# Kernel optimization log

Measured on AMD Instinct MI355X. Metric: run time of the kernel, lower is better.

Reference implementation:

```python
import jax, jax.numpy as jnp
import numpy as np
from jax import lax

N = 32768      # total nodes (8 graphs x 4096)
E = 262144     # edges (avg degree 8)
B = 8          # graphs in batch
TW = 25        # time window
H = 128        # hidden features
L = 6          # GNN layers
NV = 1         # n_variables (pos_t only)
SD = 1         # spatial dim
TMAX, TMIN, RES_T = 4.0, 0.0, 250.0
BD_LOW, BD_UP = 0.0, 16.0
EPS = 1e-5


def swish(x):
    return x * jax.nn.sigmoid(x)


def setup_inputs() -> dict:
    key = jax.random.key(0)
    ks = jax.random.split(key, 32)
    s = 0.05
    u = jax.random.normal(ks[0], (N, TW), jnp.float32)
    pos_t = jax.random.uniform(ks[1], (N, 1), jnp.float32) * TMAX
    pos_x = jax.random.uniform(ks[2], (N, 1), jnp.float32) * BD_UP
    pos = jnp.concatenate([pos_t, pos_x], axis=-1)
    edge_index = jax.random.randint(ks[3], (2, E), 0, N, jnp.int64)
    batch = jnp.repeat(jnp.arange(B, dtype=jnp.int64), N // B)
    d_in = TW + SD + NV          # 27
    d_msg = 2 * H + TW + SD + NV  # 282
    d_upd = H + H + NV            # 257
    We1 = jax.random.normal(ks[4], (d_in, H), jnp.float32) * s
    be1 = jnp.zeros((H,), jnp.float32)
    We2 = jax.random.normal(ks[5], (H, H), jnp.float32) * s
    be2 = jnp.zeros((H,), jnp.float32)
    Wm1 = jax.random.normal(ks[6], (L, d_msg, H), jnp.float32) * s
    bm1 = jnp.zeros((L, H), jnp.float32)
    Wm2 = jax.random.normal(ks[7], (L, H, H), jnp.float32) * s
    bm2 = jnp.zeros((L, H), jnp.float32)
    Wu1 = jax.random.normal(ks[8], (L, d_upd, H), jnp.float32) * s
    bu1 = jnp.zeros((L, H), jnp.float32)
    Wu2 = jax.random.normal(ks[9], (L, H, H), jnp.float32) * s
    bu2 = jnp.zeros((L, H), jnp.float32)
    Wc1 = jax.random.normal(ks[10], (8, 1, 16), jnp.float32) * s  # OIH
    bc1 = jnp.zeros((8,), jnp.float32)
    Wc2 = jax.random.normal(ks[11], (1, 8, 14), jnp.float32) * s
    bc2 = jnp.zeros((1,), jnp.float32)
    return dict(u=u, pos=pos, edge_index=edge_index, batch=batch,
                We1=We1, be1=be1, We2=We2, be2=be2,
                Wm1=Wm1, bm1=bm1, Wm2=Wm2, bm2=bm2,
                Wu1=Wu1, bu1=bu1, Wu2=Wu2, bu2=bu2,
                Wc1=Wc1, bc1=bc1, Wc2=Wc2, bc2=bc2)


def _mpnn(u, pos, edge_index, batch, We1, be1, We2, be2,
          Wm1, bm1, Wm2, bm2, Wu1, bu1, Wu2, bu2, Wc1, bc1, Wc2, bc2):
    src = edge_index[0]   # j (source)
    tgt = edge_index[1]   # i (target)
    pos_t = pos[:, 0:1] / TMAX
    pos_x = (pos[:, 1:] - BD_LOW) / (BD_UP - BD_LOW)
    variables = pos_t  # eq_variables empty -> only normalized time

    node_input = jnp.concatenate([u, pos_x, variables], axis=-1)  # [N, 27]
    h = swish(node_input @ We1 + be1)
    h = swish(h @ We2 + be2)

    # in-degree for scatter-mean (empty targets -> 0 like PyG mean)
    cnt = jnp.zeros((N,), jnp.float32).at[tgt].add(1.0)
    cnt = jnp.maximum(cnt, 1.0)[:, None]
    # per-graph node counts for InstanceNorm
    gcnt = jax.ops.segment_sum(jnp.ones((N,), jnp.float32), batch, num_segments=B)[:, None]

    u_diff_e = u[tgt] - u[src]          # [E, TW]
    p_diff_e = pos_x[tgt] - pos_x[src]  # [E, SD]
    var_i_e = variables[tgt]            # [E, NV]

    for l in range(L):
        # message: gather -> MLP per edge
        m_in = jnp.concatenate([h[tgt], h[src], u_diff_e, p_diff_e, var_i_e], axis=-1)  # [E, 282]
        msg = swish(m_in @ Wm1[l] + bm1[l])
        msg = swish(msg @ Wm2[l] + bm2[l])
        # scatter-mean aggregate onto targets
        agg = jax.ops.segment_sum(msg, tgt, num_segments=N) / cnt  # [N, H]
        # node update MLP, residual (in_features == out_features)
        up = jnp.concatenate([h, agg, variables], axis=-1)  # [N, 257]
        up = swish(up @ Wu1[l] + bu1[l])
        up = swish(up @ Wu2[l] + bu2[l])
        h = h + up
        # InstanceNorm per graph (no affine), biased variance
        mean = jax.ops.segment_sum(h, batch, num_segments=B) / gcnt      # [B, H]
        sq = jax.ops.segment_sum(h * h, batch, num_segments=B) / gcnt    # [B, H]
        var = sq - mean * mean
        h = (h - mean[batch]) / jnp.sqrt(var[batch] + EPS)

    # output CNN: tw=25 branch
    hc = h[:, None, :]  # [N, 1, 128]
    dn = ('NCH', 'OIH', 'NCH')
    c = lax.conv_general_dilated(hc, Wc1, (3,), 'VALID', dimension_numbers=dn) + bc1[None, :, None]
    c = swish(c)
    c = lax.conv_general_dilated(c, Wc2, (1,), 'VALID', dimension_numbers=dn) + bc2[None, :, None]
    diff = c[:, 0, :]  # [N, 25]

    dt = (TMAX - TMIN) / RES_T
    dt_cum = jnp.arange(1, TW + 1, dtype=jnp.float32) * dt  # cumsum of ones*dt
    out = u[:, -1:] + dt_cum[None, :] * diff
    return out


def reference(u, pos, edge_index, batch, We1, be1, We2, be2,
              Wm1, bm1, Wm2, bm2, Wu1, bu1, Wu2, bu2, Wc1, bc1, Wc2, bc2):
    return _mpnn(u, pos, edge_index, batch, We1, be1, We2, be2,
                 Wm1, bm1, Wm2, bm2, Wu1, bu1, Wu2, bu2, Wc1, bc1, Wc2, bc2)
```

## Files before the change

kernel.cpp:

```cpp
#include <hip/hip_runtime.h>
#include <stdint.h>

#define N_NODES 32768
#define N_EDGES 262144
#define NB 8
#define TW 25

typedef __attribute__((ext_vector_type(8))) short short8;
typedef __attribute__((ext_vector_type(4))) float floatx4;

__device__ __forceinline__ float swishf(float x) { return x / (1.0f + __expf(-x)); }

__device__ __forceinline__ unsigned short f2bf(float x) {
    union { float f; unsigned u; } v; v.f = x;
    unsigned r = v.u + 0x7FFFu + ((v.u >> 16) & 1u);
    return (unsigned short)(r >> 16);
}
__device__ __forceinline__ float bf2f(unsigned short b) {
    union { unsigned u; float f; } v; v.u = ((unsigned)b) << 16; return v.f;
}

__global__ void init_kernel(const float* __restrict__ pos,
                            float* __restrict__ posx, float* __restrict__ post) {
    int i = blockIdx.x * 256 + threadIdx.x;
    if (i < N_NODES) {
        post[i] = pos[i * 2 + 0] * 0.25f;
        posx[i] = pos[i * 2 + 1] * 0.0625f;
    }
}

__global__ void deg_kernel(const int* __restrict__ tgt, int* __restrict__ deg) {
    int i = blockIdx.x * 256 + threadIdx.x;
    if (i < N_EDGES) atomicAdd(&deg[tgt[i]], 1);
}

__global__ __launch_bounds__(1024) void scan_kernel(const int* __restrict__ deg,
                                                    int* __restrict__ cursor) {
    __shared__ int ps[1024];
    int t = threadIdx.x;
    int base = t * 32;
    int tot = 0;
    for (int i = 0; i < 32; ++i) tot += deg[base + i];
    ps[t] = tot;
    __syncthreads();
    for (int off = 1; off < 1024; off <<= 1) {
        int v = (t >= off) ? ps[t - off] : 0;
        __syncthreads();
        ps[t] += v;
        __syncthreads();
    }
    int run = ps[t] - tot;
    for (int i = 0; i < 32; ++i) {
        cursor[base + i] = run;
        run += deg[base + i];
    }
}

__global__ void scatter_kernel(const int* __restrict__ src, const int* __restrict__ tgt,
                               int* __restrict__ cursor,
                               int* __restrict__ src_s, int* __restrict__ tgt_s) {
    int i = blockIdx.x * 256 + threadIdx.x;
    if (i < N_EDGES) {
        int tg = tgt[i];
        int p = atomicAdd(&cursor[tg], 1);
        src_s[p] = src[i];
        tgt_s[p] = tg;
    }
}

__global__ __launch_bounds__(256) void ediff_kernel(
    const float* __restrict__ u, const float* __restrict__ posx,
    const float* __restrict__ post,
    const int* __restrict__ src_s, const int* __restrict__ tgt_s,
    unsigned short* __restrict__ ediff)
{
    int e = blockIdx.x * 256 + threadIdx.x;
    if (e >= N_EDGES) return;
    int s = src_s[e], g = tgt_s[e];
    unsigned short buf[32];
    #pragma unroll
    for (int k = 0; k < 25; ++k)
        buf[k] = f2bf(u[(size_t)g * 25 + k] - u[(size_t)s * 25 + k]);
    buf[25] = f2bf(posx[g] - posx[s]);
    buf[26] = f2bf(post[g]);
    #pragma unroll
    for (int k = 27; k < 32; ++k) buf[k] = 0;
    #pragma unroll
    for (int j = 0; j < 4; ++j)
        *(short8*)(ediff + (size_t)e * 32 + j * 8) = *(short8*)&buf[j * 8];
}

__global__ __launch_bounds__(256) void pack_kernel(const float* __restrict__ W,
                                                   unsigned short* __restrict__ Wp,
                                                   int Kreal, int Kc, int total) {
    int id = blockIdx.x * 256 + threadIdx.x;
    if (id >= total) return;
    int lane = id & 63;
    int t8 = (id >> 6) & 7;
    int rest = id >> 9;
    int c = rest % Kc;
    int l = rest / Kc;
    int n = t8 * 16 + (lane & 15);
    int kb = c * 32 + (lane >> 4) * 8;
    short8 v;
    #pragma unroll
    for (int j = 0; j < 8; ++j) {
        int k = kb + j;
        float x = (k < Kreal) ? W[((size_t)l * Kreal + k) * 128 + n] : 0.f;
        v[j] = (short)f2bf(x);
    }
    *(short8*)(Wp + (size_t)id * 8) = v;
}

__global__ __launch_bounds__(256) void encoder_kernel(
    const float* __restrict__ u, const float* __restrict__ posx,
    const float* __restrict__ post,
    const float* __restrict__ We1, const float* __restrict__ be1,
    const float* __restrict__ We2, const float* __restrict__ be2,
    float* __restrict__ h, unsigned short* __restrict__ h_bf,
    float* __restrict__ agg)
{
    __shared__ __align__(16) float As[64 * 36];
    __shared__ __align__(16) float Ws[32 * 128];
    __shared__ __align__(16) float Ms[64 * 128];

    int t = threadIdx.x;
    int n0 = blockIdx.x * 64;
    int rg = t >> 5, cg = t & 31;

    {
        int r = t & 63, cseg = t >> 6;
        float4 z = make_float4(0.f, 0.f, 0.f, 0.f);
        #pragma unroll
        for (int j = 0; j < 8; ++j)
            *(float4*)(agg + (size_t)(n0 + r) * 128 + cseg * 32 + j * 4) = z;
    }

    float acc[8][4] = {};
    {
        int kk = t >> 3, cb = (t & 7) * 16;
        #pragma unroll
        for (int j = 0; j < 4; ++j) {
            float4 w = make_float4(0.f, 0.f, 0.f, 0.f);
            if (kk < 27) w = *(const float4*)&We1[kk * 128 + cb + j * 4];
            *(float4*)&Ws[kk * 128 + cb + j * 4] = w;
        }
        int el = t >> 2, kb = (t & 3) * 8, n = n0 + el;
        float v[8];
        #pragma unroll
        for (int j = 0; j < 8; ++j) {
            int k = kb + j;
            float x = 0.f;
            if (k < 25) x = u[n * 25 + k];
            else if (k == 25) x = posx[n];
            else if (k == 26) x = post[n];
            v[j] = x;
        }
        #pragma unroll
        for (int j = 0; j < 8; j += 4)
            *(float4*)&As[el * 36 + kb + j] = make_float4(v[j], v[j+1], v[j+2], v[j+3]);
        __syncthreads();
        #pragma unroll 4
        for (int kk2 = 0; kk2 < 32; ++kk2) {
            float4 b = *(const float4*)&Ws[kk2 * 128 + cg * 4];
            float a[8];
            #pragma unroll
            for (int i = 0; i < 8; ++i) a[i] = As[(rg * 8 + i) * 36 + kk2];
            #pragma unroll
            for (int i = 0; i < 8; ++i) {
                acc[i][0] += a[i] * b.x; acc[i][1] += a[i] * b.y;
                acc[i][2] += a[i] * b.z; acc[i][3] += a[i] * b.w;
            }
        }
        __syncthreads();
    }
    {
        float4 b1 = *(const float4*)&be1[cg * 4];
        #pragma unroll
        for (int i = 0; i < 8; ++i) {
            float4 m;
            m.x = swishf(acc[i][0] + b1.x);
            m.y = swishf(acc[i][1] + b1.y);
            m.z = swishf(acc[i][2] + b1.z);
            m.w = swishf(acc[i][3] + b1.w);
            *(float4*)&Ms[(rg * 8 + i) * 128 + cg * 4] = m;
        }
        __syncthreads();
    }
    float acc2[8][4] = {};
    for (int k0 = 0; k0 < 128; k0 += 32) {
        int kk = t >> 3, cb = (t & 7) * 16;
        #pragma unroll
        for (int j = 0; j < 4; ++j)
            *(float4*)&Ws[kk * 128 + cb + j * 4] =
                *(const float4*)&We2[(k0 + kk) * 128 + cb + j * 4];
        __syncthreads();
        #pragma unroll 4
        for (int kk2 = 0; kk2 < 32; ++kk2) {
            float4 b = *(const float4*)&Ws[kk2 * 128 + cg * 4];
            float a[8];
            #pragma unroll
            for (int i = 0; i < 8; ++i) a[i] = Ms[(rg * 8 + i) * 128 + (k0 + kk2)];
            #pragma unroll
            for (int i = 0; i < 8; ++i) {
                acc2[i][0] += a[i] * b.x; acc2[i][1] += a[i] * b.y;
                acc2[i][2] += a[i] * b.z; acc2[i][3] += a[i] * b.w;
            }
        }
        __syncthreads();
    }
    {
        float4 b2 = *(const float4*)&be2[cg * 4];
        #pragma unroll
        for (int i = 0; i < 8; ++i) {
            int n = n0 + rg * 8 + i;
            float4 o;
            o.x = swishf(acc2[i][0] + b2.x);
            o.y = swishf(acc2[i][1] + b2.y);
            o.z = swishf(acc2[i][2] + b2.z);
            o.w = swishf(acc2[i][3] + b2.w);
            *(float4*)&h[(size_t)n * 128 + cg * 4] = o;
            unsigned short* hb = h_bf + (size_t)n * 128 + cg * 4;
            uint2 pk;
            pk.x = (unsigned)f2bf(o.x) | ((unsigned)f2bf(o.y) << 16);
            pk.y = (unsigned)f2bf(o.z) | ((unsigned)f2bf(o.w) << 16);
            *(uint2*)hb = pk;
        }
    }
}

__global__ __launch_bounds__(256, 4) void message_kernel(
    const unsigned short* __restrict__ h_bf,
    const unsigned short* __restrict__ ediff,
    const int* __restrict__ src_s, const int* __restrict__ tgt_s,
    const unsigned short* __restrict__ W1p, const float* __restrict__ b1,
    const unsigned short* __restrict__ W2p, const float* __restrict__ b2,
    float* __restrict__ agg, float* __restrict__ stats)
{
    __shared__ __align__(16) unsigned short SH[64 * 296];
    __shared__ int tgtS[64];
    unsigned short* Msh = SH;
    unsigned short* Cs  = SH + 9216;

    int t = threadIdx.x;
    int e0 = blockIdx.x * 64;
    if (blockIdx.x == 0) {
        float4 z = make_float4(0.f, 0.f, 0.f, 0.f);
        *(float4*)&stats[t * 8] = z;
        *(float4*)&stats[t * 8 + 4] = z;
    }
    if (t < 64) tgtS[t] = tgt_s[e0 + t];

    {
        int r = t & 63, cseg = t >> 6;
        int g = tgt_s[e0 + r], s = src_s[e0 + r];
        const short8* hg = (const short8*)(h_bf + (size_t)g * 128);
        const short8* hs = (const short8*)(h_bf + (size_t)s * 128);
        #pragma unroll
        for (int j = 0; j < 4; ++j) {
            int chunk = cseg * 4 + j;
            *(short8*)(SH + r * 296 + chunk * 8)       = hg[chunk];
            *(short8*)(SH + r * 296 + 128 + chunk * 8) = hs[chunk];
        }
        *(short8*)(SH + r * 296 + 256 + cseg * 8) =
            *(const short8*)(ediff + (size_t)(e0 + r) * 32 + cseg * 8);
    }
    __syncthreads();

    int w = t >> 6, lane = t & 63, q = lane >> 4, m = lane & 15;
    int t80 = 2 * w, t81 = 2 * w + 1;

    floatx4 acc0[4] = {}, acc1[4] = {};
    #pragma unroll
    for (int c = 0; c < 9; ++c) {
        short8 b0 = *(const short8*)(W1p + ((size_t)(c * 8 + t80) * 64 + lane) * 8);
        short8 b1f = *(const short8*)(W1p + ((size_t)(c * 8 + t81) * 64 + lane) * 8);
        #pragma unroll
        for (int g2 = 0; g2 < 4; ++g2) {
            short8 a = *(const short8*)(SH + (g2 * 16 + m) * 296 + c * 32 + q * 8);
            acc0[g2] = __builtin_amdgcn_mfma_f32_16x16x32_bf16(a, b0, acc0[g2], 0, 0, 0);
            acc1[g2] = __builtin_amdgcn_mfma_f32_16x16x32_bf16(a, b1f, acc1[g2], 0, 0, 0);
        }
    }
    __syncthreads();

    {
        float bv0 = b1[t80 * 16 + m], bv1 = b1[t81 * 16 + m];
        #pragma unroll
        for (int g2 = 0; g2 < 4; ++g2) {
            #pragma unroll
            for (int r = 0; r < 4; ++r) {
                int row = g2 * 16 + q * 4 + r;
                Msh[row * 136 + t80 * 16 + m] = f2bf(swishf(acc0[g2][r] + bv0));
                Msh[row * 136 + t81 * 16 + m] = f2bf(swishf(acc1[g2][r] + bv1));
            }
        }
    }
    __syncthreads();

    floatx4 acc2a[4] = {}, acc2b[4] = {};
    #pragma unroll
    for (int c = 0; c < 4; ++c) {
        short8 b0 = *(const short8*)(W2p + ((size_t)(c * 8 + t80) * 64 + lane) * 8);
        short8 b1f = *(const short8*)(W2p + ((size_t)(c * 8 + t81) * 64 + lane) * 8);
        #pragma unroll
        for (int g2 = 0; g2 < 4; ++g2) {
            short8 a = *(const short8*)(Msh + (g2 * 16 + m) * 136 + c * 32 + q * 8);
            acc2a[g2] = __builtin_amdgcn_mfma_f32_16x16x32_bf16(a, b0, acc2a[g2], 0, 0, 0);
            acc2b[g2] = __builtin_amdgcn_mfma_f32_16x16x32_bf16(a, b1f, acc2b[g2], 0, 0, 0);
        }
    }
    {
        float bv0 = b2[t80 * 16 + m], bv1 = b2[t81 * 16 + m];
        #pragma unroll
        for (int g2 = 0; g2 < 4; ++g2) {
            #pragma unroll
            for (int r = 0; r < 4; ++r) {
                int row = g2 * 16 + q * 4 + r;
                Cs[row * 132 + t80 * 16 + m] = f2bf(swishf(acc2a[g2][r] + bv0));
                Cs[row * 132 + t81 * 16 + m] = f2bf(swishf(acc2b[g2][r] + bv1));
            }
        }
    }
    __syncthreads();

    {
        int col = t & 127, half = t >> 7;
        int r0 = half * 32;
        float run = 0.f;
        int prev = tgtS[r0];
        bool atStart = true;
        for (int i = 0; i < 32; ++i) {
            int tg = tgtS[r0 + i];
            if (tg != prev) {
                float* dst = &agg[(size_t)prev * 128 + col];
                if (atStart) atomicAdd(dst, run);
                else *dst = run;
                run = 0.f; prev = tg; atStart = false;
            }
            run += bf2f(Cs[(r0 + i) * 132 + col]);
        }
        atomicAdd(&agg[(size_t)prev * 128 + col], run);
    }
}

__global__ __launch_bounds__(256, 2) void update_kernel(
    float* __restrict__ h, const unsigned short* __restrict__ h_bf,
    float* __restrict__ agg, const int* __restrict__ deg,
    const float* __restrict__ post,
    const unsigned short* __restrict__ W1p, const float* __restrict__ b1,
    const unsigned short* __restrict__ W2p, const float* __restrict__ b2,
    float* __restrict__ stats)
{
    __shared__ __align__(16) unsigned short SH[64 * 296];
    unsigned short* Msh = SH;

    int t = threadIdx.x;
    int n0 = blockIdx.x * 64;

    {
        int r = t & 63, cseg = t >> 6;
        int n = n0 + r;
        const short8* hn = (const short8*)(h_bf + (size_t)n * 128);
        #pragma unroll
        for (int j = 0; j < 4; ++j) {
            int chunk = cseg * 4 + j;
            *(short8*)(SH + r * 296 + chunk * 8) = hn[chunk];
        }
        float ic = 1.0f / fmaxf((float)deg[n], 1.0f);
        #pragma unroll
        for (int j = 0; j < 4; ++j) {
            int unit = cseg * 4 + j;
            const float* ap = agg + (size_t)n * 128 + unit * 8;
            float4 v0 = *(const float4*)ap;
            float4 v1 = *(const float4*)(ap + 4);
            short8 a;
            a[0] = (short)f2bf(v0.x * ic); a[1] = (short)f2bf(v0.y * ic);
            a[2] = (short)f2bf(v0.z * ic); a[3] = (short)f2bf(v0.w * ic);
            a[4] = (short)f2bf(v1.x * ic); a[5] = (short)f2bf(v1.y * ic);
            a[6] = (short)f2bf(v1.z * ic); a[7] = (short)f2bf(v1.w * ic);
            *(short8*)(SH + r * 296 + 128 + unit * 8) = a;
        }
        short8 z;
        #pragma unroll
        for (int k = 0; k < 8; ++k) z[k] = 0;
        if (cseg == 0) z[0] = (short)f2bf(post[n]);
        *(short8*)(SH + r * 296 + 256 + cseg * 8) = z;
    }
    __syncthreads();

    int w = t >> 6, lane = t & 63, q = lane >> 4, m = lane & 15;
    int t80 = 2 * w, t81 = 2 * w + 1;

    floatx4 acc0[4] = {}, acc1[4] = {};
    #pragma unroll
    for (int c = 0; c < 9; ++c) {
        short8 b0 = *(const short8*)(W1p + ((size_t)(c * 8 + t80) * 64 + lane) * 8);
        short8 b1f = *(const short8*)(W1p + ((size_t)(c * 8 + t81) * 64 + lane) * 8);
        #pragma unroll
        for (int g2 = 0; g2 < 4; ++g2) {
            short8 a = *(const short8*)(SH + (g2 * 16 + m) * 296 + c * 32 + q * 8);
            acc0[g2] = __builtin_amdgcn_mfma_f32_16x16x32_bf16(a, b0, acc0[g2], 0, 0, 0);
            acc1[g2] = __builtin_amdgcn_mfma_f32_16x16x32_bf16(a, b1f, acc1[g2], 0, 0, 0);
        }
    }
    __syncthreads();

    {
        float bv0 = b1[t80 * 16 + m], bv1 = b1[t81 * 16 + m];
        #pragma unroll
        for (int g2 = 0; g2 < 4; ++g2) {
            #pragma unroll
            for (int r = 0; r < 4; ++r) {
                int row = g2 * 16 + q * 4 + r;
                Msh[row * 136 + t80 * 16 + m] = f2bf(swishf(acc0[g2][r] + bv0));
                Msh[row * 136 + t81 * 16 + m] = f2bf(swishf(acc1[g2][r] + bv1));
            }
        }
    }
    __syncthreads();

    floatx4 acc2a[4] = {}, acc2b[4] = {};
    #pragma unroll
    for (int c = 0; c < 4; ++c) {
        short8 b0 = *(const short8*)(W2p + ((size_t)(c * 8 + t80) * 64 + lane) * 8);
        short8 b1f = *(const short8*)(W2p + ((size_t)(c * 8 + t81) * 64 + lane) * 8);
        #pragma unroll
        for (int g2 = 0; g2 < 4; ++g2) {
            short8 a = *(const short8*)(Msh + (g2 * 16 + m) * 136 + c * 32 + q * 8);
            acc2a[g2] = __builtin_amdgcn_mfma_f32_16x16x32_bf16(a, b0, acc2a[g2], 0, 0, 0);
            acc2b[g2] = __builtin_amdgcn_mfma_f32_16x16x32_bf16(a, b1f, acc2b[g2], 0, 0, 0);
        }
    }

    int bidx = n0 >> 12;
    int col0 = t80 * 16 + m, col1 = t81 * 16 + m;
    float bv0 = b2[col0], bv1 = b2[col1];
    float s0 = 0.f, s20 = 0.f, s1 = 0.f, s21 = 0.f;
    #pragma unroll
    for (int g2 = 0; g2 < 4; ++g2) {
        #pragma unroll
        for (int r = 0; r < 4; ++r) {
            int row = g2 * 16 + q * 4 + r;
            size_t i0 = (size_t)(n0 + row) * 128 + col0;
            size_t i1 = (size_t)(n0 + row) * 128 + col1;
            float hv0 = h[i0] + swishf(acc2a[g2][r] + bv0);
            float hv1 = h[i1] + swishf(acc2b[g2][r] + bv1);
            h[i0] = hv0; h[i1] = hv1;
            s0 += hv0; s20 += hv0 * hv0;
            s1 += hv1; s21 += hv1 * hv1;
        }
    }
    s0  += __shfl_xor(s0, 16);  s0  += __shfl_xor(s0, 32);
    s20 += __shfl_xor(s20, 16); s20 += __shfl_xor(s20, 32);
    s1  += __shfl_xor(s1, 16);  s1  += __shfl_xor(s1, 32);
    s21 += __shfl_xor(s21, 16); s21 += __shfl_xor(s21, 32);
    if (q == 0) {
        atomicAdd(&stats[bidx * 128 + col0], s0);
        atomicAdd(&stats[(NB + bidx) * 128 + col0], s20);
        atomicAdd(&stats[bidx * 128 + col1], s1);
        atomicAdd(&stats[(NB + bidx) * 128 + col1], s21);
    }
    {
        int r = t & 63, cseg = t >> 6;
        float4 z = make_float4(0.f, 0.f, 0.f, 0.f);
        #pragma unroll
        for (int j = 0; j < 8; ++j)
            *(float4*)(agg + (size_t)(n0 + r) * 128 + cseg * 32 + j * 4) = z;
    }
}

__global__ __launch_bounds__(256) void norm_kernel(float* __restrict__ h,
                                                   unsigned short* __restrict__ h_bf,
                                                   const float* __restrict__ stats) {
    size_t id = (size_t)blockIdx.x * 256 + threadIdx.x;
    int n = (int)(id >> 5), c4 = (int)(id & 31) * 4;
    int b = n >> 12;
    float4 mn = *(const float4*)&stats[b * 128 + c4];
    float4 sq = *(const float4*)&stats[(NB + b) * 128 + c4];
    float4 v = *(const float4*)&h[(size_t)n * 128 + c4];
    float4 r;
    float m0 = mn.x * (1.f / 4096.f), m1 = mn.y * (1.f / 4096.f);
    float m2 = mn.z * (1.f / 4096.f), m3 = mn.w * (1.f / 4096.f);
    r.x = (v.x - m0) * rsqrtf(sq.x * (1.f / 4096.f) - m0 * m0 + 1e-5f);
    r.y = (v.y - m1) * rsqrtf(sq.y * (1.f / 4096.f) - m1 * m1 + 1e-5f);
    r.z = (v.z - m2) * rsqrtf(sq.z * (1.f / 4096.f) - m2 * m2 + 1e-5f);
    r.w = (v.w - m3) * rsqrtf(sq.w * (1.f / 4096.f) - m3 * m3 + 1e-5f);
    *(float4*)&h[(size_t)n * 128 + c4] = r;
    uint2 pk;
    pk.x = (unsigned)f2bf(r.x) | ((unsigned)f2bf(r.y) << 16);
    pk.y = (unsigned)f2bf(r.z) | ((unsigned)f2bf(r.w) << 16);
    *(uint2*)(h_bf + (size_t)n * 128 + c4) = pk;
}

__global__ __launch_bounds__(256) void conv_kernel(
    const float* __restrict__ h, const float* __restrict__ u,
    const float* __restrict__ Wc1, const float* __restrict__ bc1,
    const float* __restrict__ Wc2, const float* __restrict__ bc2,
    float* __restrict__ out)
{
    __shared__ float hs[4][128];
    __shared__ float c1[4][8 * 40];
    int w = threadIdx.x >> 6, lane = threadIdx.x & 63;
    int n = blockIdx.x * 4 + w;
    hs[w][lane] = h[(size_t)n * 128 + lane];
    hs[w][lane + 64] = h[(size_t)n * 128 + lane + 64];
    __syncthreads();
    for (int idx = lane; idx < 304; idx += 64) {
        int o = idx / 38, p = idx % 38;
        float s = bc1[o];
        #pragma unroll
        for (int k = 0; k < 16; ++k) s += hs[w][p * 3 + k] * Wc1[o * 16 + k];
        c1[w][o * 40 + p] = swishf(s);
    }
    __syncthreads();
    if (lane < TW) {
        float s = bc2[0];
        #pragma unroll
        for (int o = 0; o < 8; ++o)
            for (int k = 0; k < 14; ++k)
                s += c1[w][o * 40 + lane + k] * Wc2[o * 14 + k];
        float dt_cum = (float)(lane + 1) * (4.0f / 250.0f);
        out[n * TW + lane] = u[n * 25 + 24] + dt_cum * s;
    }
}

extern "C" void kernel_launch(void* const* d_in, const int* in_sizes, int n_in,
                              void* d_out, int out_size, void* d_ws, size_t ws_size,
                              hipStream_t stream)
{
    const float* u   = (const float*)d_in[0];
    const float* pos = (const float*)d_in[1];
    const int*   ei  = (const int*)d_in[2];
    const float* We1 = (const float*)d_in[4];
    const float* be1 = (const float*)d_in[5];
    const float* We2 = (const float*)d_in[6];
    const float* be2 = (const float*)d_in[7];
    const float* Wm1 = (const float*)d_in[8];
    const float* bm1 = (const float*)d_in[9];
    const float* Wm2 = (const float*)d_in[10];
    const float* bm2 = (const float*)d_in[11];
    const float* Wu1 = (const float*)d_in[12];
    const float* bu1 = (const float*)d_in[13];
    const float* Wu2 = (const float*)d_in[14];
    const float* bu2 = (const float*)d_in[15];
    const float* Wc1 = (const float*)d_in[16];
    const float* bc1 = (const float*)d_in[17];
    const float* Wc2 = (const float*)d_in[18];
    const float* bc2 = (const float*)d_in[19];
    float* out = (float*)d_out;

    char* base = (char*)d_ws;
    size_t off = 0;
    auto alloc = [&](size_t bytes) -> char* {
        char* r = base + off;
        off = (off + bytes + 511) & ~(size_t)511;
        return r;
    };
    float*          h      = (float*)alloc((size_t)N_NODES * 128 * 4);
    unsigned short* h_bf   = (unsigned short*)alloc((size_t)N_NODES * 128 * 2);
    float*          agg    = (float*)alloc((size_t)N_NODES * 128 * 4);
    float*          posx   = (float*)alloc(N_NODES * 4);
    float*          post   = (float*)alloc(N_NODES * 4);
    float*          stats  = (float*)alloc(2 * NB * 128 * 4);
    int*            deg    = (int*)alloc(N_NODES * 4);
    int*            cursor = (int*)alloc(N_NODES * 4);
    int*            src_s  = (int*)alloc((size_t)N_EDGES * 4);
    int*            tgt_s  = (int*)alloc((size_t)N_EDGES * 4);
    unsigned short* ediff  = (unsigned short*)alloc((size_t)N_EDGES * 32 * 2);
    unsigned short* Wm1p   = (unsigned short*)alloc((size_t)6 * 9 * 4096 * 2);
    unsigned short* Wm2p   = (unsigned short*)alloc((size_t)6 * 4 * 4096 * 2);
    unsigned short* Wu1p   = (unsigned short*)alloc((size_t)6 * 9 * 4096 * 2);
    unsigned short* Wu2p   = (unsigned short*)alloc((size_t)6 * 4 * 4096 * 2);
    (void)ws_size;

    const int* srcp = ei;
    const int* tgtp = ei + N_EDGES;

    init_kernel<<<N_NODES / 256, 256, 0, stream>>>(pos, posx, post);
    hipMemsetAsync(deg, 0, N_NODES * sizeof(int), stream);
    deg_kernel<<<N_EDGES / 256, 256, 0, stream>>>(tgtp, deg);
    scan_kernel<<<1, 1024, 0, stream>>>(deg, cursor);
    scatter_kernel<<<N_EDGES / 256, 256, 0, stream>>>(srcp, tgtp, cursor, src_s, tgt_s);
    ediff_kernel<<<N_EDGES / 256, 256, 0, stream>>>(u, posx, post, src_s, tgt_s, ediff);
    encoder_kernel<<<N_NODES / 64, 256, 0, stream>>>(u, posx, post, We1, be1, We2, be2,
                                                     h, h_bf, agg);
    {
        int tot1 = 6 * 9 * 512;
        int tot2 = 6 * 4 * 512;
        pack_kernel<<<(tot1 + 255) / 256, 256, 0, stream>>>(Wm1, Wm1p, 283, 9, tot1);
        pack_kernel<<<(tot2 + 255) / 256, 256, 0, stream>>>(Wm2, Wm2p, 128, 4, tot2);
        pack_kernel<<<(tot1 + 255) / 256, 256, 0, stream>>>(Wu1, Wu1p, 257, 9, tot1);
        pack_kernel<<<(tot2 + 255) / 256, 256, 0, stream>>>(Wu2, Wu2p, 128, 4, tot2);
    }

    for (int l = 0; l < 6; ++l) {
        message_kernel<<<N_EDGES / 64, 256, 0, stream>>>(
            h_bf, ediff, src_s, tgt_s,
            Wm1p + (size_t)l * 9 * 4096, bm1 + l * 128,
            Wm2p + (size_t)l * 4 * 4096, bm2 + l * 128, agg, stats);
        update_kernel<<<N_NODES / 64, 256, 0, stream>>>(
            h, h_bf, agg, deg, post,
            Wu1p + (size_t)l * 9 * 4096, bu1 + l * 128,
            Wu2p + (size_t)l * 4 * 4096, bu2 + l * 128, stats);
        norm_kernel<<<(N_NODES * 32) / 256, 256, 0, stream>>>(h, h_bf, stats);
    }

    conv_kernel<<<N_NODES / 4, 256, 0, stream>>>(h, u, Wc1, bc1, Wc2, bc2, out);
}
```

Before: 769.6 us.

## Double message/update block tile to 128 rows with 512 threads

The message and update kernels now process 128 edges or nodes per block with 8 waves instead of 64 with 4. Each wave owns one 16-column output tile across 8 row groups instead of two column tiles across 4 row groups. LDS moves to a dynamic allocation sized for the larger tile. This halves per-row weight-fragment global loads and block count, but doubles LDS A-fragment reads per MFMA and raises LDS per block, which may cap occupancy.

```diff
diff --git a/kernel.cpp b/kernel.cpp
--- a/kernel.cpp
+++ b/kernel.cpp
@@ -229,7 +229,7 @@
     }
 }
 
-__global__ __launch_bounds__(256, 4) void message_kernel(
+__global__ __launch_bounds__(512, 4) void message_kernel(
     const unsigned short* __restrict__ h_bf,
     const unsigned short* __restrict__ ediff,
     const int* __restrict__ src_s, const int* __restrict__ tgt_s,
@@ -237,22 +237,22 @@
     const unsigned short* __restrict__ W2p, const float* __restrict__ b2,
     float* __restrict__ agg, float* __restrict__ stats)
 {
-    __shared__ __align__(16) unsigned short SH[64 * 296];
-    __shared__ int tgtS[64];
+    extern __shared__ __align__(16) unsigned short SH[];
+    __shared__ int tgtS[128];
     unsigned short* Msh = SH;
-    unsigned short* Cs  = SH + 9216;
+    unsigned short* Cs  = SH + 17408;
 
     int t = threadIdx.x;
-    int e0 = blockIdx.x * 64;
-    if (blockIdx.x == 0) {
+    int e0 = blockIdx.x * 128;
+    if (blockIdx.x == 0 && t < 256) {
         float4 z = make_float4(0.f, 0.f, 0.f, 0.f);
         *(float4*)&stats[t * 8] = z;
         *(float4*)&stats[t * 8 + 4] = z;
     }
-    if (t < 64) tgtS[t] = tgt_s[e0 + t];
-
-    {
-        int r = t & 63, cseg = t >> 6;
+    if (t < 128) tgtS[t] = tgt_s[e0 + t];
+
+    {
+        int r = t & 127, cseg = t >> 7;
         int g = tgt_s[e0 + r], s = src_s[e0 + r];
         const short8* hg = (const short8*)(h_bf + (size_t)g * 128);
         const short8* hs = (const short8*)(h_bf + (size_t)s * 128);
@@ -268,65 +268,58 @@
     __syncthreads();
 
     int w = t >> 6, lane = t & 63, q = lane >> 4, m = lane & 15;
-    int t80 = 2 * w, t81 = 2 * w + 1;
-
-    floatx4 acc0[4] = {}, acc1[4] = {};
+
+    floatx4 acc[8] = {};
     #pragma unroll
     for (int c = 0; c < 9; ++c) {
-        short8 b0 = *(const short8*)(W1p + ((size_t)(c * 8 + t80) * 64 + lane) * 8);
-        short8 b1f = *(const short8*)(W1p + ((size_t)(c * 8 + t81) * 64 + lane) * 8);
-        #pragma unroll
-        for (int g2 = 0; g2 < 4; ++g2) {
+        short8 b = *(const short8*)(W1p + ((size_t)(c * 8 + w) * 64 + lane) * 8);
+        #pragma unroll
+        for (int g2 = 0; g2 < 8; ++g2) {
             short8 a = *(const short8*)(SH + (g2 * 16 + m) * 296 + c * 32 + q * 8);
-            acc0[g2] = __builtin_amdgcn_mfma_f32_16x16x32_bf16(a, b0, acc0[g2], 0, 0, 0);
-            acc1[g2] = __builtin_amdgcn_mfma_f32_16x16x32_bf16(a, b1f, acc1[g2], 0, 0, 0);
-        }
-    }
-    __syncthreads();
-
-    {
-        float bv0 = b1[t80 * 16 + m], bv1 = b1[t81 * 16 + m];
-        #pragma unroll
-        for (int g2 = 0; g2 < 4; ++g2) {
+            acc[g2] = __builtin_amdgcn_mfma_f32_16x16x32_bf16(a, b, acc[g2], 0, 0, 0);
+        }
+    }
+    __syncthreads();
+
+    {
+        float bv = b1[w * 16 + m];
+        #pragma unroll
+        for (int g2 = 0; g2 < 8; ++g2) {
             #pragma unroll
             for (int r = 0; r < 4; ++r) {
                 int row = g2 * 16 + q * 4 + r;
-                Msh[row * 136 + t80 * 16 + m] = f2bf(swishf(acc0[g2][r] + bv0));
-                Msh[row * 136 + t81 * 16 + m] = f2bf(swishf(acc1[g2][r] + bv1));
+                Msh[row * 136 + w * 16 + m] = f2bf(swishf(acc[g2][r] + bv));
             }
         }
     }
     __syncthreads();
 
-    floatx4 acc2a[4] = {}, acc2b[4] = {};
+    floatx4 acc2[8] = {};
     #pragma unroll
     for (int c = 0; c < 4; ++c) {
-        short8 b0 = *(const short8*)(W2p + ((size_t)(c * 8 + t80) * 64 + lane) * 8);
-        short8 b1f = *(const short8*)(W2p + ((size_t)(c * 8 + t81) * 64 + lane) * 8);
-        #pragma unroll
-        for (int g2 = 0; g2 < 4; ++g2) {
+        short8 b = *(const short8*)(W2p + ((size_t)(c * 8 + w) * 64 + lane) * 8);
+        #pragma unroll
+        for (int g2 = 0; g2 < 8; ++g2) {
             short8 a = *(const short8*)(Msh + (g2 * 16 + m) * 136 + c * 32 + q * 8);
-            acc2a[g2] = __builtin_amdgcn_mfma_f32_16x16x32_bf16(a, b0, acc2a[g2], 0, 0, 0);
-            acc2b[g2] = __builtin_amdgcn_mfma_f32_16x16x32_bf16(a, b1f, acc2b[g2], 0, 0, 0);
-        }
-    }
-    {
-        float bv0 = b2[t80 * 16 + m], bv1 = b2[t81 * 16 + m];
-        #pragma unroll
-        for (int g2 = 0; g2 < 4; ++g2) {
+            acc2[g2] = __builtin_amdgcn_mfma_f32_16x16x32_bf16(a, b, acc2[g2], 0, 0, 0);
+        }
+    }
+    {
+        float bv = b2[w * 16 + m];
+        #pragma unroll
+        for (int g2 = 0; g2 < 8; ++g2) {
             #pragma unroll
             for (int r = 0; r < 4; ++r) {
                 int row = g2 * 16 + q * 4 + r;
-                Cs[row * 132 + t80 * 16 + m] = f2bf(swishf(acc2a[g2][r] + bv0));
-                Cs[row * 132 + t81 * 16 + m] = f2bf(swishf(acc2b[g2][r] + bv1));
+                Cs[row * 132 + w * 16 + m] = f2bf(swishf(acc2[g2][r] + bv));
             }
         }
     }
     __syncthreads();
 
     {
-        int col = t & 127, half = t >> 7;
-        int r0 = half * 32;
+        int col = t & 127, quarter = t >> 7;
+        int r0 = quarter * 32;
         float run = 0.f;
         int prev = tgtS[r0];
         bool atStart = true;
@@ -344,7 +337,7 @@
     }
 }
 
-__global__ __launch_bounds__(256, 2) void update_kernel(
+__global__ __launch_bounds__(512, 4) void update_kernel(
     float* __restrict__ h, const unsigned short* __restrict__ h_bf,
     float* __restrict__ agg, const int* __restrict__ deg,
     const float* __restrict__ post,
@@ -352,14 +345,14 @@
     const unsigned short* __restrict__ W2p, const float* __restrict__ b2,
     float* __restrict__ stats)
 {
-    __shared__ __align__(16) unsigned short SH[64 * 296];
+    extern __shared__ __align__(16) unsigned short SH[];
     unsigned short* Msh = SH;
 
     int t = threadIdx.x;
-    int n0 = blockIdx.x * 64;
-
-    {
-        int r = t & 63, cseg = t >> 6;
+    int n0 = blockIdx.x * 128;
+
+    {
+        int r = t & 127, cseg = t >> 7;
         int n = n0 + r;
         const short8* hn = (const short8*)(h_bf + (size_t)n * 128);
         #pragma unroll
@@ -390,79 +383,66 @@
     __syncthreads();
 
     int w = t >> 6, lane = t & 63, q = lane >> 4, m = lane & 15;
-    int t80 = 2 * w, t81 = 2 * w + 1;
-
-    floatx4 acc0[4] = {}, acc1[4] = {};
+
+    floatx4 acc[8] = {};
     #pragma unroll
     for (int c = 0; c < 9; ++c) {
-        short8 b0 = *(const short8*)(W1p + ((size_t)(c * 8 + t80) * 64 + lane) * 8);
-        short8 b1f = *(const short8*)(W1p + ((size_t)(c * 8 + t81) * 64 + lane) * 8);
-        #pragma unroll
-        for (int g2 = 0; g2 < 4; ++g2) {
+        short8 b = *(const short8*)(W1p + ((size_t)(c * 8 + w) * 64 + lane) * 8);
+        #pragma unroll
+        for (int g2 = 0; g2 < 8; ++g2) {
             short8 a = *(const short8*)(SH + (g2 * 16 + m) * 296 + c * 32 + q * 8);
-            acc0[g2] = __builtin_amdgcn_mfma_f32_16x16x32_bf16(a, b0, acc0[g2], 0, 0, 0);
-            acc1[g2] = __builtin_amdgcn_mfma_f32_16x16x32_bf16(a, b1f, acc1[g2], 0, 0, 0);
-        }
-    }
-    __syncthreads();
-
-    {
-        float bv0 = b1[t80 * 16 + m], bv1 = b1[t81 * 16 + m];
-        #pragma unroll
-        for (int g2 = 0; g2 < 4; ++g2) {
+            acc[g2] = __builtin_amdgcn_mfma_f32_16x16x32_bf16(a, b, acc[g2], 0, 0, 0);
+        }
+    }
+    __syncthreads();
+
+    {
+        float bv = b1[w * 16 + m];
+        #pragma unroll
+        for (int g2 = 0; g2 < 8; ++g2) {
             #pragma unroll
             for (int r = 0; r < 4; ++r) {
                 int row = g2 * 16 + q * 4 + r;
-                Msh[row * 136 + t80 * 16 + m] = f2bf(swishf(acc0[g2][r] + bv0));
-                Msh[row * 136 + t81 * 16 + m] = f2bf(swishf(acc1[g2][r] + bv1));
+                Msh[row * 136 + w * 16 + m] = f2bf(swishf(acc[g2][r] + bv));
             }
         }
     }
     __syncthreads();
 
-    floatx4 acc2a[4] = {}, acc2b[4] = {};
+    floatx4 acc2[8] = {};
     #pragma unroll
     for (int c = 0; c < 4; ++c) {
-        short8 b0 = *(const short8*)(W2p + ((size_t)(c * 8 + t80) * 64 + lane) * 8);
-        short8 b1f = *(const short8*)(W2p + ((size_t)(c * 8 + t81) * 64 + lane) * 8);
-        #pragma unroll
-        for (int g2 = 0; g2 < 4; ++g2) {
+        short8 b = *(const short8*)(W2p + ((size_t)(c * 8 + w) * 64 + lane) * 8);
+        #pragma unroll
+        for (int g2 = 0; g2 < 8; ++g2) {
             short8 a = *(const short8*)(Msh + (g2 * 16 + m) * 136 + c * 32 + q * 8);
-            acc2a[g2] = __builtin_amdgcn_mfma_f32_16x16x32_bf16(a, b0, acc2a[g2], 0, 0, 0);
-            acc2b[g2] = __builtin_amdgcn_mfma_f32_16x16x32_bf16(a, b1f, acc2b[g2], 0, 0, 0);
+            acc2[g2] = __builtin_amdgcn_mfma_f32_16x16x32_bf16(a, b, acc2[g2], 0, 0, 0);
         }
     }
 
     int bidx = n0 >> 12;
-    int col0 = t80 * 16 + m, col1 = t81 * 16 + m;
-    float bv0 = b2[col0], bv1 = b2[col1];
-    float s0 = 0.f, s20 = 0.f, s1 = 0.f, s21 = 0.f;
-    #pragma unroll
-    for (int g2 = 0; g2 < 4; ++g2) {
+    int col = w * 16 + m;
+    float bv = b2[col];
+    float s = 0.f, s2 = 0.f;
+    #pragma unroll
+    for (int g2 = 0; g2 < 8; ++g2) {
         #pragma unroll
         for (int r = 0; r < 4; ++r) {
             int row = g2 * 16 + q * 4 + r;
-            size_t i0 = (size_t)(n0 + row) * 128 + col0;
-            size_t i1 = (size_t)(n0 + row) * 128 + col1;
-            float hv0 = h[i0] + swishf(acc2a[g2][r] + bv0);
-            float hv1 = h[i1] + swishf(acc2b[g2][r] + bv1);
-            h[i0] = hv0; h[i1] = hv1;
-            s0 += hv0; s20 += hv0 * hv0;
-            s1 += hv1; s21 += hv1 * hv1;
-        }
-    }
-    s0  += __shfl_xor(s0, 16);  s0  += __shfl_xor(s0, 32);
-    s20 += __shfl_xor(s20, 16); s20 += __shfl_xor(s20, 32);
-    s1  += __shfl_xor(s1, 16);  s1  += __shfl_xor(s1, 32);
-    s21 += __shfl_xor(s21, 16); s21 += __shfl_xor(s21, 32);
+            size_t i0 = (size_t)(n0 + row) * 128 + col;
+            float hv = h[i0] + swishf(acc2[g2][r] + bv);
+            h[i0] = hv;
+            s += hv; s2 += hv * hv;
+        }
+    }
+    s  += __shfl_xor(s, 16);  s  += __shfl_xor(s, 32);
+    s2 += __shfl_xor(s2, 16); s2 += __shfl_xor(s2, 32);
     if (q == 0) {
-        atomicAdd(&stats[bidx * 128 + col0], s0);
-        atomicAdd(&stats[(NB + bidx) * 128 + col0], s20);
-        atomicAdd(&stats[bidx * 128 + col1], s1);
-        atomicAdd(&stats[(NB + bidx) * 128 + col1], s21);
-    }
-    {
-        int r = t & 63, cseg = t >> 6;
+        atomicAdd(&stats[bidx * 128 + col], s);
+        atomicAdd(&stats[(NB + bidx) * 128 + col], s2);
+    }
+    {
+        int r = t & 127, cseg = t >> 7;
         float4 z = make_float4(0.f, 0.f, 0.f, 0.f);
         #pragma unroll
         for (int j = 0; j < 8; ++j)
@@ -577,6 +557,12 @@
     const int* srcp = ei;
     const int* tgtp = ei + N_EDGES;
 
+    const int dynLds = 128 * 296 * 2;
+    hipFuncSetAttribute((const void*)message_kernel,
+                        hipFuncAttributeMaxDynamicSharedMemorySize, dynLds);
+    hipFuncSetAttribute((const void*)update_kernel,
+                        hipFuncAttributeMaxDynamicSharedMemorySize, dynLds);
+
     init_kernel<<<N_NODES / 256, 256, 0, stream>>>(pos, posx, post);
     hipMemsetAsync(deg, 0, N_NODES * sizeof(int), stream);
     deg_kernel<<<N_EDGES / 256, 256, 0, stream>>>(tgtp, deg);
@@ -595,11 +581,11 @@
     }
 
     for (int l = 0; l < 6; ++l) {
-        message_kernel<<<N_EDGES / 64, 256, 0, stream>>>(
+        message_kernel<<<N_EDGES / 128, 512, dynLds, stream>>>(
             h_bf, ediff, src_s, tgt_s,
             Wm1p + (size_t)l * 9 * 4096, bm1 + l * 128,
             Wm2p + (size_t)l * 4 * 4096, bm2 + l * 128, agg, stats);
-        update_kernel<<<N_NODES / 64, 256, 0, stream>>>(
+        update_kernel<<<N_NODES / 128, 512, dynLds, stream>>>(
             h, h_bf, agg, deg, post,
             Wu1p + (size_t)l * 9 * 4096, bu1 + l * 128,
             Wu2p + (size_t)l * 4 * 4096, bu2 + l * 128, stats);
```

New measurement: 791.3 us. +2.8%, slower.

## Use 8 waves per message block, one 16-column tile per wave

Applied to the files above, without the earlier changes.

Expands the message kernel from 4 to 8 wavefronts per 64-edge block. Each wave now computes a single 16-column output tile instead of two, and the gather loop is split across more threads. The aim is more latency hiding and lower per-thread register pressure. In exchange it adds per-block sync cost, and the final aggregation leaves half the threads idle.

```diff
diff --git a/kernel.cpp b/kernel.cpp
--- a/kernel.cpp
+++ b/kernel.cpp
@@ -229,7 +229,7 @@
     }
 }
 
-__global__ __launch_bounds__(256, 4) void message_kernel(
+__global__ __launch_bounds__(512, 8) void message_kernel(
     const unsigned short* __restrict__ h_bf,
     const unsigned short* __restrict__ ediff,
     const int* __restrict__ src_s, const int* __restrict__ tgt_s,
@@ -244,7 +244,7 @@
 
     int t = threadIdx.x;
     int e0 = blockIdx.x * 64;
-    if (blockIdx.x == 0) {
+    if (blockIdx.x == 0 && t < 256) {
         float4 z = make_float4(0.f, 0.f, 0.f, 0.f);
         *(float4*)&stats[t * 8] = z;
         *(float4*)&stats[t * 8 + 4] = z;
@@ -257,74 +257,68 @@
         const short8* hg = (const short8*)(h_bf + (size_t)g * 128);
         const short8* hs = (const short8*)(h_bf + (size_t)s * 128);
         #pragma unroll
-        for (int j = 0; j < 4; ++j) {
-            int chunk = cseg * 4 + j;
+        for (int j = 0; j < 2; ++j) {
+            int chunk = cseg * 2 + j;
             *(short8*)(SH + r * 296 + chunk * 8)       = hg[chunk];
             *(short8*)(SH + r * 296 + 128 + chunk * 8) = hs[chunk];
         }
-        *(short8*)(SH + r * 296 + 256 + cseg * 8) =
-            *(const short8*)(ediff + (size_t)(e0 + r) * 32 + cseg * 8);
+        if (cseg < 4)
+            *(short8*)(SH + r * 296 + 256 + cseg * 8) =
+                *(const short8*)(ediff + (size_t)(e0 + r) * 32 + cseg * 8);
     }
     __syncthreads();
 
     int w = t >> 6, lane = t & 63, q = lane >> 4, m = lane & 15;
-    int t80 = 2 * w, t81 = 2 * w + 1;
-
-    floatx4 acc0[4] = {}, acc1[4] = {};
+
+    floatx4 acc[4] = {};
     #pragma unroll
     for (int c = 0; c < 9; ++c) {
-        short8 b0 = *(const short8*)(W1p + ((size_t)(c * 8 + t80) * 64 + lane) * 8);
-        short8 b1f = *(const short8*)(W1p + ((size_t)(c * 8 + t81) * 64 + lane) * 8);
+        short8 b = *(const short8*)(W1p + ((size_t)(c * 8 + w) * 64 + lane) * 8);
         #pragma unroll
         for (int g2 = 0; g2 < 4; ++g2) {
             short8 a = *(const short8*)(SH + (g2 * 16 + m) * 296 + c * 32 + q * 8);
-            acc0[g2] = __builtin_amdgcn_mfma_f32_16x16x32_bf16(a, b0, acc0[g2], 0, 0, 0);
-            acc1[g2] = __builtin_amdgcn_mfma_f32_16x16x32_bf16(a, b1f, acc1[g2], 0, 0, 0);
-        }
-    }
-    __syncthreads();
-
-    {
-        float bv0 = b1[t80 * 16 + m], bv1 = b1[t81 * 16 + m];
+            acc[g2] = __builtin_amdgcn_mfma_f32_16x16x32_bf16(a, b, acc[g2], 0, 0, 0);
+        }
+    }
+    __syncthreads();
+
+    {
+        float bv = b1[w * 16 + m];
         #pragma unroll
         for (int g2 = 0; g2 < 4; ++g2) {
             #pragma unroll
             for (int r = 0; r < 4; ++r) {
                 int row = g2 * 16 + q * 4 + r;
-                Msh[row * 136 + t80 * 16 + m] = f2bf(swishf(acc0[g2][r] + bv0));
-                Msh[row * 136 + t81 * 16 + m] = f2bf(swishf(acc1[g2][r] + bv1));
+                Msh[row * 136 + w * 16 + m] = f2bf(swishf(acc[g2][r] + bv));
             }
         }
     }
     __syncthreads();
 
-    floatx4 acc2a[4] = {}, acc2b[4] = {};
+    floatx4 acc2[4] = {};
     #pragma unroll
     for (int c = 0; c < 4; ++c) {
-        short8 b0 = *(const short8*)(W2p + ((size_t)(c * 8 + t80) * 64 + lane) * 8);
-        short8 b1f = *(const short8*)(W2p + ((size_t)(c * 8 + t81) * 64 + lane) * 8);
+        short8 b = *(const short8*)(W2p + ((size_t)(c * 8 + w) * 64 + lane) * 8);
         #pragma unroll
         for (int g2 = 0; g2 < 4; ++g2) {
             short8 a = *(const short8*)(Msh + (g2 * 16 + m) * 136 + c * 32 + q * 8);
-            acc2a[g2] = __builtin_amdgcn_mfma_f32_16x16x32_bf16(a, b0, acc2a[g2], 0, 0, 0);
-            acc2b[g2] = __builtin_amdgcn_mfma_f32_16x16x32_bf16(a, b1f, acc2b[g2], 0, 0, 0);
-        }
-    }
-    {
-        float bv0 = b2[t80 * 16 + m], bv1 = b2[t81 * 16 + m];
+            acc2[g2] = __builtin_amdgcn_mfma_f32_16x16x32_bf16(a, b, acc2[g2], 0, 0, 0);
+        }
+    }
+    {
+        float bv = b2[w * 16 + m];
         #pragma unroll
         for (int g2 = 0; g2 < 4; ++g2) {
             #pragma unroll
             for (int r = 0; r < 4; ++r) {
                 int row = g2 * 16 + q * 4 + r;
-                Cs[row * 132 + t80 * 16 + m] = f2bf(swishf(acc2a[g2][r] + bv0));
-                Cs[row * 132 + t81 * 16 + m] = f2bf(swishf(acc2b[g2][r] + bv1));
+                Cs[row * 132 + w * 16 + m] = f2bf(swishf(acc2[g2][r] + bv));
             }
         }
     }
     __syncthreads();
 
-    {
+    if (t < 256) {
         int col = t & 127, half = t >> 7;
         int r0 = half * 32;
         float run = 0.f;
@@ -595,7 +589,7 @@
     }
 
     for (int l = 0; l < 6; ++l) {
-        message_kernel<<<N_EDGES / 64, 256, 0, stream>>>(
+        message_kernel<<<N_EDGES / 64, 512, 0, stream>>>(
             h_bf, ediff, src_s, tgt_s,
             Wm1p + (size_t)l * 9 * 4096, bm1 + l * 128,
             Wm2p + (size_t)l * 4 * 4096, bm2 + l * 128, agg, stats);
```

Result: faster. 745.6 us (-3.1%).
